# Performance work log

Hardware: AMD Instinct MI355X
Metric: run time of the kernel (lower is better)

Reference implementation:

```python
import jax, jax.numpy as jnp
import numpy as np

EMBED_DIM = 1024
NUM_HEADS = 16
HEAD_DIM = EMBED_DIM // NUM_HEADS
FF_DIM = 4 * EMBED_DIM
LN_EPS = 1e-5


def _layernorm(x, g, b):
    mu = jnp.mean(x, axis=-1, keepdims=True)
    var = jnp.var(x, axis=-1, keepdims=True)
    return (x - mu) * jax.lax.rsqrt(var + LN_EPS) * g + b


def setup_inputs() -> dict:
    key = jax.random.key(0)
    ks = jax.random.split(key, 8)
    B, T, C = 2, 2048, EMBED_DIM
    s_c = 1.0 / np.sqrt(C)
    s_f = 1.0 / np.sqrt(FF_DIM)
    return {
        "x": jax.random.normal(ks[0], (B, T, C), jnp.float32),
        "ln1_g": jnp.ones((C,), jnp.float32),
        "ln1_b": jnp.zeros((C,), jnp.float32),
        "qkv_w": jax.random.uniform(ks[1], (C, 3 * C), jnp.float32, -s_c, s_c),
        "qkv_b": jnp.zeros((3 * C,), jnp.float32),
        "out_w": jax.random.uniform(ks[2], (C, C), jnp.float32, -s_c, s_c),
        "out_b": jnp.zeros((C,), jnp.float32),
        "ln2_g": jnp.ones((C,), jnp.float32),
        "ln2_b": jnp.zeros((C,), jnp.float32),
        "ff1_w": jax.random.uniform(ks[3], (C, FF_DIM), jnp.float32, -s_c, s_c),
        "ff1_b": jnp.zeros((FF_DIM,), jnp.float32),
        "ff2_w": jax.random.uniform(ks[4], (FF_DIM, C), jnp.float32, -s_f, s_f),
        "ff2_b": jnp.zeros((C,), jnp.float32),
    }


def reference(x, ln1_g, ln1_b, qkv_w, qkv_b, out_w, out_b,
              ln2_g, ln2_b, ff1_w, ff1_b, ff2_w, ff2_b):
    B, T, C = x.shape
    H, D = NUM_HEADS, HEAD_DIM

    # --- pre-LN causal self-attention ---
    h = _layernorm(x, ln1_g, ln1_b)
    qkv = h @ qkv_w + qkv_b                      # [B,T,3C]
    q, k, v = jnp.split(qkv, 3, axis=-1)
    q = q.reshape(B, T, H, D)
    k = k.reshape(B, T, H, D)
    v = v.reshape(B, T, H, D)
    scores = jnp.einsum('bqhd,bkhd->bhqk', q, k) / np.sqrt(D)  # [B,H,T,T]
    causal = jnp.tril(jnp.ones((T, T), bool))
    scores = jnp.where(causal, scores, -jnp.inf)
    attn = jax.nn.softmax(scores, axis=-1)
    o = jnp.einsum('bhqk,bkhd->bqhd', attn, v).reshape(B, T, C)
    x = x + o @ out_w + out_b

    # --- GELU MLP ---
    h2 = _layernorm(x, ln2_g, ln2_b)
    ff = jax.nn.gelu(h2 @ ff1_w + ff1_b, approximate=False) @ ff2_w + ff2_b
    return x + ff
```

## Files before the change

### kernel.cpp

```cpp
#include <hip/hip_runtime.h>
#include <hip/hip_bf16.h>
#include <math.h>

#define B_ 2
#define T_ 2048
#define C_ 1024
#define H_ 16
#define D_ 64
#define F_ 4096
#define BT_ (B_*T_)

typedef __attribute__((ext_vector_type(8))) short bf16x8;
typedef __attribute__((ext_vector_type(4))) float f32x4;

__device__ __forceinline__ float bfraw2f(unsigned int u){
    union { unsigned int i; float f; } c; c.i = u << 16; return c.f;
}
__device__ __forceinline__ short f2bfraw(float f){
    union { float f; unsigned int i; } c; c.f = f;
    unsigned int u = c.i;
    u += 0x7fffu + ((u >> 16) & 1u);
    return (short)(u >> 16);
}
__device__ __forceinline__ void gl2lds16(const void* g, void* l) {
    __builtin_amdgcn_global_load_lds(
        (const __attribute__((address_space(1))) unsigned int*)g,
        (__attribute__((address_space(3))) unsigned int*)l,
        16, 0, 0);
}

__global__ __launch_bounds__(256) void wconv_t(const float* __restrict__ W,
                                               short* __restrict__ Wt,
                                               int K, int N)
{
    __shared__ short tile[64][65];
    int k0 = blockIdx.y * 64, n0 = blockIdx.x * 64;
    int t = threadIdx.x;
#pragma unroll
    for (int i = 0; i < 4; i++) {
        int idx = t + i * 256;
        int r = idx >> 4, c4 = (idx & 15) * 4;
        float4 u = *(const float4*)(W + (size_t)(k0 + r) * N + n0 + c4);
        tile[c4 + 0][r] = f2bfraw(u.x);
        tile[c4 + 1][r] = f2bfraw(u.y);
        tile[c4 + 2][r] = f2bfraw(u.z);
        tile[c4 + 3][r] = f2bfraw(u.w);
    }
    __syncthreads();
#pragma unroll
    for (int i = 0; i < 2; i++) {
        int idx = t + i * 256;
        int r = idx >> 3, c8 = (idx & 7) * 8;
        short v[8];
#pragma unroll
        for (int u8 = 0; u8 < 8; u8++) v[u8] = tile[r][c8 + u8];
        *(uint4*)(Wt + (size_t)(n0 + r) * K + k0 + c8) = *(const uint4*)v;
    }
}

__global__ __launch_bounds__(256) void v_transpose(const __hip_bfloat16* __restrict__ qkv,
                                                   short* __restrict__ vt)
{
    __shared__ short tile[64][65];
    int kb = blockIdx.x * 64;
    int h = blockIdx.y, b = blockIdx.z;
    const short* src = (const short*)qkv + (size_t)b * T_ * 3 * C_ + 2 * C_ + h * D_;
    int t = threadIdx.x;
#pragma unroll
    for (int i = 0; i < 2; i++) {
        int idx = t + i * 256;
        int r = idx >> 3, c8 = (idx & 7) * 8;
        bf16x8 v = *(const bf16x8*)(src + (size_t)(kb + r) * 3 * C_ + c8);
#pragma unroll
        for (int u = 0; u < 8; u++) tile[c8 + u][r] = v[u];
    }
    __syncthreads();
    short* dst = vt + (size_t)(b * H_ + h) * D_ * T_ + kb;
#pragma unroll
    for (int i = 0; i < 2; i++) {
        int idx = t + i * 256;
        int r = idx >> 3, c8 = (idx & 7) * 8;
        short v[8];
#pragma unroll
        for (int u = 0; u < 8; u++) v[u] = tile[r][c8 + u];
        *(uint4*)(dst + (size_t)r * T_ + c8) = *(const uint4*)v;
    }
}

__global__ __launch_bounds__(256) void ln_fused(const float* __restrict__ x, int ldx,
                                                const float* __restrict__ g,
                                                const float* __restrict__ b,
                                                __hip_bfloat16* out, int ldo)
{
    __shared__ float sm1[4], sm2[4];
    __shared__ float smu, srs;
    int row = blockIdx.x, t = threadIdx.x;
    const float* xr = x + (size_t)row * ldx;
    float v[4]; float s = 0.f, ss = 0.f;
#pragma unroll
    for (int i = 0; i < 4; i++) {
        float f = xr[t + i * 256];
        v[i] = f; s += f; ss += f * f;
    }
#pragma unroll
    for (int off = 32; off >= 1; off >>= 1) {
        s  += __shfl_xor(s,  off);
        ss += __shfl_xor(ss, off);
    }
    int wave = t >> 6, lane = t & 63;
    if (!lane) { sm1[wave] = s; sm2[wave] = ss; }
    __syncthreads();
    if (t == 0) {
        s  = sm1[0] + sm1[1] + sm1[2] + sm1[3];
        ss = sm2[0] + sm2[1] + sm2[2] + sm2[3];
        float mu  = s * (1.f / C_);
        float var = ss * (1.f / C_) - mu * mu;
        if (var < 0.f) var = 0.f;
        smu = mu; srs = rsqrtf(var + 1e-5f);
    }
    __syncthreads();
    float mu = smu, rs = srs;
#pragma unroll
    for (int i = 0; i < 4; i++) {
        int c = t + i * 256;
        out[(size_t)row * ldo + c] = __float2bfloat16((v[i] - mu) * rs * g[c] + b[c]);
    }
}

template<int ACT>
__global__ __launch_bounds__(256) void gemm128(
    const __hip_bfloat16* A, int lda,
    const short* Wt, int ldw, int noff, int koff,
    const float* __restrict__ bias, int boff,
    void* out, int ldo,
    int K)
{
    __shared__ __align__(16) short As[2][128 * 32];
    __shared__ __align__(16) short Bs[2][128 * 32];
    int tid = threadIdx.x;
    int w = tid >> 6, lane = tid & 63;
    int quad = lane >> 4, l16 = lane & 15;
    int wm = w >> 1, wn = w & 1;
    int m0 = blockIdx.y * 128, n0 = blockIdx.x * 128;
    int lr = lane >> 2, lk = (lane & 3) * 8;

    const __hip_bfloat16* Ag = A + (size_t)(m0 + w * 32 + lr) * lda + lk;
    const short*          Bg = Wt + (size_t)(noff + n0 + w * 32 + lr) * ldw + koff + lk;

    f32x4 acc[4][4];
#pragma unroll
    for (int i = 0; i < 4; i++)
#pragma unroll
        for (int j = 0; j < 4; j++) acc[i][j] = (f32x4){0.f, 0.f, 0.f, 0.f};

    gl2lds16(Ag,            &As[0][(w * 32) * 32]);
    gl2lds16(Ag + 16 * lda, &As[0][(w * 32 + 16) * 32]);
    gl2lds16(Bg,            &Bs[0][(w * 32) * 32]);
    gl2lds16(Bg + 16 * ldw, &Bs[0][(w * 32 + 16) * 32]);
    __syncthreads();

    int cur = 0;
    for (int k0 = 0; k0 < K; k0 += 32) {
        if (k0 + 32 < K) {
            int kn = k0 + 32, nb = cur ^ 1;
            gl2lds16(Ag + kn,            &As[nb][(w * 32) * 32]);
            gl2lds16(Ag + 16 * lda + kn, &As[nb][(w * 32 + 16) * 32]);
            gl2lds16(Bg + kn,            &Bs[nb][(w * 32) * 32]);
            gl2lds16(Bg + 16 * ldw + kn, &Bs[nb][(w * 32 + 16) * 32]);
        }
        bf16x8 af[4], bfr[4];
#pragma unroll
        for (int mt = 0; mt < 4; mt++)
            af[mt] = *(const bf16x8*)&As[cur][(wm * 64 + mt * 16 + l16) * 32 + quad * 8];
#pragma unroll
        for (int nt = 0; nt < 4; nt++)
            bfr[nt] = *(const bf16x8*)&Bs[cur][(wn * 64 + nt * 16 + l16) * 32 + quad * 8];
#pragma unroll
        for (int mt = 0; mt < 4; mt++)
#pragma unroll
            for (int nt = 0; nt < 4; nt++)
                acc[mt][nt] = __builtin_amdgcn_mfma_f32_16x16x32_bf16(af[mt], bfr[nt], acc[mt][nt], 0, 0, 0);
        __syncthreads();
        cur ^= 1;
    }

#pragma unroll
    for (int nt = 0; nt < 4; nt++) {
        int c = n0 + wn * 64 + nt * 16 + l16;
        float bv = bias ? bias[boff + c] : 0.f;
#pragma unroll
        for (int mt = 0; mt < 4; mt++) {
#pragma unroll
            for (int reg = 0; reg < 4; reg++) {
                int r = m0 + wm * 64 + mt * 16 + quad * 4 + reg;
                float v = acc[mt][nt][reg] + bv;
                if (ACT == 1) v = 0.5f * v * (1.f + erff(v * 0.70710678118654752f));
                ((__hip_bfloat16*)out)[(size_t)r * ldo + c] = __float2bfloat16(v);
            }
        }
    }
}

__global__ __launch_bounds__(256) void gemm64n(
    const __hip_bfloat16* A, int lda,
    const short* Wt, int ldw, int koff,
    const float* __restrict__ bias,
    const float* res, int ldres,
    float* out, int ldo,
    int K)
{
    __shared__ __align__(16) short As[2][128 * 32];
    __shared__ __align__(16) short Bs[2][64 * 32];
    int tid = threadIdx.x;
    int w = tid >> 6, lane = tid & 63;
    int quad = lane >> 4, l16 = lane & 15;
    int wm = w >> 1, wn = w & 1;
    int m0 = blockIdx.y * 128, n0 = blockIdx.x * 64;
    int lr = lane >> 2, lk = (lane & 3) * 8;

    const __hip_bfloat16* Ag = A + (size_t)(m0 + w * 32 + lr) * lda + lk;
    const short*          Bg = Wt + (size_t)(n0 + w * 16 + lr) * ldw + koff + lk;

    f32x4 acc[4][2];
#pragma unroll
    for (int i = 0; i < 4; i++)
#pragma unroll
        for (int j = 0; j < 2; j++) acc[i][j] = (f32x4){0.f, 0.f, 0.f, 0.f};

    gl2lds16(Ag,            &As[0][(w * 32) * 32]);
    gl2lds16(Ag + 16 * lda, &As[0][(w * 32 + 16) * 32]);
    gl2lds16(Bg,            &Bs[0][(w * 16) * 32]);
    __syncthreads();

    int cur = 0;
    for (int k0 = 0; k0 < K; k0 += 32) {
        if (k0 + 32 < K) {
            int kn = k0 + 32, nb = cur ^ 1;
            gl2lds16(Ag + kn,            &As[nb][(w * 32) * 32]);
            gl2lds16(Ag + 16 * lda + kn, &As[nb][(w * 32 + 16) * 32]);
            gl2lds16(Bg + kn,            &Bs[nb][(w * 16) * 32]);
        }
        bf16x8 af[4], bfr[2];
#pragma unroll
        for (int mt = 0; mt < 4; mt++)
            af[mt] = *(const bf16x8*)&As[cur][(wm * 64 + mt * 16 + l16) * 32 + quad * 8];
#pragma unroll
        for (int nt = 0; nt < 2; nt++)
            bfr[nt] = *(const bf16x8*)&Bs[cur][(wn * 32 + nt * 16 + l16) * 32 + quad * 8];
#pragma unroll
        for (int mt = 0; mt < 4; mt++)
#pragma unroll
            for (int nt = 0; nt < 2; nt++)
                acc[mt][nt] = __builtin_amdgcn_mfma_f32_16x16x32_bf16(af[mt], bfr[nt], acc[mt][nt], 0, 0, 0);
        __syncthreads();
        cur ^= 1;
    }

#pragma unroll
    for (int nt = 0; nt < 2; nt++) {
        int c = n0 + wn * 32 + nt * 16 + l16;
        float bv = bias ? bias[c] : 0.f;
#pragma unroll
        for (int mt = 0; mt < 4; mt++) {
#pragma unroll
            for (int reg = 0; reg < 4; reg++) {
                int r = m0 + wm * 64 + mt * 16 + quad * 4 + reg;
                float v = acc[mt][nt][reg] + bv + res[(size_t)r * ldres + c];
                out[(size_t)r * ldo + c] = v;
            }
        }
    }
}

__global__ __launch_bounds__(256, 2) void attn_flash(__hip_bfloat16* qkv,
                                                     const short* __restrict__ vt)
{
    __shared__ __align__(16) short Ks[2][64 * 64];
    __shared__ __align__(16) short Vs[2][64 * 64];
    __shared__ __align__(16) short Pl[4][16 * 72];
    int tid = threadIdx.x;
    int wave = tid >> 6, lane = tid & 63;
    int quad = lane >> 4, l16 = lane & 15;
    int fid = blockIdx.x + 16 * blockIdx.y;
    int h = (fid & 7) * 2 + ((fid >> 3) >> 4);
    int i = (fid >> 3) & 15;
    int b = blockIdx.z;
    int qbs[2]; qbs[0] = i; qbs[1] = 31 - i;
    const size_t rs = 3 * C_;
    __hip_bfloat16* base = qkv + (size_t)b * T_ * rs;
    const __hip_bfloat16* Qb = base + h * D_;
    const __hip_bfloat16* Kb = base + C_ + h * D_;
    const short* Vt = vt + (size_t)(b * H_ + h) * D_ * T_;

    bf16x8 qf[2][2];
#pragma unroll
    for (int tq = 0; tq < 2; tq++) {
        const __hip_bfloat16* qr = Qb + (size_t)(qbs[tq] * 64 + wave * 16 + l16) * rs + quad * 8;
        qf[tq][0] = *(const bf16x8*)qr;
        qf[tq][1] = *(const bf16x8*)(qr + 32);
    }

    f32x4 o[2][4];
    float m[2][4], l[2][4];
#pragma unroll
    for (int tq = 0; tq < 2; tq++)
#pragma unroll
        for (int t = 0; t < 4; t++) {
            o[tq][t] = (f32x4){0.f, 0.f, 0.f, 0.f};
            m[tq][t] = -INFINITY;
            l[tq][t] = 0.f;
        }
    short* Pw = &Pl[wave][0];

    int srow = wave * 16 + (lane >> 3);
    int scg  = ((lane & 7) ^ (lane >> 3)) * 8;
    const __hip_bfloat16* Kg = Kb + (size_t)srow * rs + scg;
    const short*          Vg = Vt + (size_t)srow * T_ + scg;

    int cur = 0;
#pragma unroll
    for (int j = 0; j < 2; j++) {
        gl2lds16(Kg + (size_t)(j * 8) * rs, &Ks[0][(wave * 2 + j) * 512]);
        gl2lds16(Vg + (size_t)(j * 8) * T_, &Vs[0][(wave * 2 + j) * 512]);
    }
    __syncthreads();

    int qhi = qbs[1];
    int swz = (l16 & 7);
    for (int kt = 0; kt <= qhi; kt++) {
        if (kt < qhi) {
            int kb = (kt + 1) * 64;
#pragma unroll
            for (int j = 0; j < 2; j++) {
                gl2lds16(Kg + (size_t)(kb + j * 8) * rs, &Ks[cur ^ 1][(wave * 2 + j) * 512]);
                gl2lds16(Vg + (size_t)(j * 8) * T_ + kb, &Vs[cur ^ 1][(wave * 2 + j) * 512]);
            }
        }
        const short* Kc = Ks[cur];
        const short* Vc = Vs[cur];
#pragma unroll
        for (int tq = 0; tq < 2; tq++) {
            if (tq == 0 && kt > qbs[0]) continue;
            f32x4 sa[4];
            __builtin_amdgcn_s_setprio(1);
#pragma unroll
            for (int t16 = 0; t16 < 4; t16++) {
                int row = t16 * 16 + l16;
                bf16x8 kf0 = *(const bf16x8*)&Kc[row * 64 + ((quad     ^ swz)) * 8];
                bf16x8 kf1 = *(const bf16x8*)&Kc[row * 64 + (((quad + 4) ^ swz)) * 8];
                f32x4 s = (f32x4){0.f, 0.f, 0.f, 0.f};
                s = __builtin_amdgcn_mfma_f32_16x16x32_bf16(qf[tq][0], kf0, s, 0, 0, 0);
                s = __builtin_amdgcn_mfma_f32_16x16x32_bf16(qf[tq][1], kf1, s, 0, 0, 0);
                sa[t16] = s;
            }
            __builtin_amdgcn_s_setprio(0);
            bool maskit = (kt == qbs[tq]);
#pragma unroll
            for (int t16 = 0; t16 < 4; t16++) {
#pragma unroll
                for (int reg = 0; reg < 4; reg++) {
                    float v = sa[t16][reg] * 0.125f;
                    if (maskit) {
                        int keyl = t16 * 16 + l16;
                        int ql = wave * 16 + quad * 4 + reg;
                        if (keyl > ql) v = -3.0e38f;
                    }
                    sa[t16][reg] = v;
                }
            }
            float mx[4];
#pragma unroll
            for (int reg = 0; reg < 4; reg++)
                mx[reg] = fmaxf(fmaxf(sa[0][reg], sa[1][reg]), fmaxf(sa[2][reg], sa[3][reg]));
#pragma unroll
            for (int off = 8; off >= 1; off >>= 1)
#pragma unroll
                for (int reg = 0; reg < 4; reg++)
                    mx[reg] = fmaxf(mx[reg], __shfl_xor(mx[reg], off));
            float alpha[4];
#pragma unroll
            for (int reg = 0; reg < 4; reg++) {
                float mn = fmaxf(m[tq][reg], mx[reg]);
                alpha[reg] = __expf(m[tq][reg] - mn);
                m[tq][reg] = mn;
            }
            float rsum[4] = {0.f, 0.f, 0.f, 0.f};
#pragma unroll
            for (int t16 = 0; t16 < 4; t16++) {
#pragma unroll
                for (int reg = 0; reg < 4; reg++) {
                    float p = __expf(sa[t16][reg] - m[tq][reg]);
                    rsum[reg] += p;
                    Pw[(quad * 4 + reg) * 72 + t16 * 16 + l16] = f2bfraw(p);
                }
            }
#pragma unroll
            for (int off = 8; off >= 1; off >>= 1)
#pragma unroll
                for (int reg = 0; reg < 4; reg++)
                    rsum[reg] += __shfl_xor(rsum[reg], off);
#pragma unroll
            for (int reg = 0; reg < 4; reg++)
                l[tq][reg] = l[tq][reg] * alpha[reg] + rsum[reg];
#pragma unroll
            for (int t = 0; t < 4; t++)
#pragma unroll
                for (int reg = 0; reg < 4; reg++)
                    o[tq][t][reg] *= alpha[reg];
            __builtin_amdgcn_s_setprio(1);
#pragma unroll
            for (int chunk = 0; chunk < 2; chunk++) {
                bf16x8 pf = *(const bf16x8*)&Pw[l16 * 72 + chunk * 32 + quad * 8];
#pragma unroll
                for (int dt = 0; dt < 4; dt++) {
                    int row = dt * 16 + l16;
                    bf16x8 vf = *(const bf16x8*)&Vc[row * 64 + (((chunk * 4 + quad) ^ swz)) * 8];
                    o[tq][dt] = __builtin_amdgcn_mfma_f32_16x16x32_bf16(pf, vf, o[tq][dt], 0, 0, 0);
                }
            }
            __builtin_amdgcn_s_setprio(0);
        }
        __syncthreads();
        cur ^= 1;
    }

#pragma unroll
    for (int tq = 0; tq < 2; tq++) {
#pragma unroll
        for (int dt = 0; dt < 4; dt++) {
#pragma unroll
            for (int reg = 0; reg < 4; reg++) {
                int r = qbs[tq] * 64 + wave * 16 + quad * 4 + reg;
                float v = o[tq][dt][reg] / l[tq][reg];
                base[(size_t)r * rs + h * D_ + dt * 16 + l16] = __float2bfloat16(v);
            }
        }
    }
}

extern "C" void kernel_launch(void* const* d_in, const int* in_sizes, int n_in,
                              void* d_out, int out_size, void* d_ws, size_t ws_size,
                              hipStream_t stream)
{
    const float* x     = (const float*)d_in[0];
    const float* ln1_g = (const float*)d_in[1];
    const float* ln1_b = (const float*)d_in[2];
    const float* qkv_w = (const float*)d_in[3];
    const float* qkv_b = (const float*)d_in[4];
    const float* out_w = (const float*)d_in[5];
    const float* out_b = (const float*)d_in[6];
    const float* ln2_g = (const float*)d_in[7];
    const float* ln2_b = (const float*)d_in[8];
    const float* ff1_w = (const float*)d_in[9];
    const float* ff1_b = (const float*)d_in[10];
    const float* ff2_w = (const float*)d_in[11];
    const float* ff2_b = (const float*)d_in[12];

    char* ws = (char*)d_ws;
    __hip_bfloat16* qkv = (__hip_bfloat16*)ws;
    short* qkvwT = (short*)(ws + 25165824);
    short* outwT = (short*)(ws + 31457280);
    short* ff1wT = (short*)(ws + 33554432);
    short* ff2wT = (short*)(ws + 41943040);
    __hip_bfloat16* hbuf2 = qkv;
    __hip_bfloat16* act   = qkv + 1024;
    __hip_bfloat16* hbuf1 = (__hip_bfloat16*)d_out;
    float* x1 = (float*)d_out;
    short* vtbuf = (short*)d_out;

    wconv_t<<<dim3(3 * C_ / 64, C_ / 64), 256, 0, stream>>>(qkv_w, qkvwT, C_, 3 * C_);
    wconv_t<<<dim3(C_ / 64, C_ / 64),     256, 0, stream>>>(out_w, outwT, C_, C_);
    wconv_t<<<dim3(F_ / 64, C_ / 64),     256, 0, stream>>>(ff1_w, ff1wT, C_, F_);
    wconv_t<<<dim3(C_ / 64, F_ / 64),     256, 0, stream>>>(ff2_w, ff2wT, F_, C_);

    ln_fused<<<BT_, 256, 0, stream>>>(x, C_, ln1_g, ln1_b, hbuf1, C_);
    gemm128<0><<<dim3(3 * C_ / 128, BT_ / 128), 256, 0, stream>>>(
        hbuf1, C_, qkvwT, C_, 0, 0, qkv_b, 0, qkv, 3 * C_, C_);
    v_transpose<<<dim3(T_ / 64, H_, B_), 256, 0, stream>>>(qkv, vtbuf);
    attn_flash<<<dim3(16, H_, B_), 256, 0, stream>>>(qkv, vtbuf);
    gemm64n<<<dim3(C_ / 64, BT_ / 128), 256, 0, stream>>>(
        qkv, 3 * C_, outwT, C_, 0, out_b, x, C_, x1, C_, C_);
    ln_fused<<<BT_, 256, 0, stream>>>(x1, C_, ln2_g, ln2_b, hbuf2, 3 * C_);
    for (int f = 0; f < 2; f++) {
        gemm128<1><<<dim3(2048 / 128, BT_ / 128), 256, 0, stream>>>(
            hbuf2, 3 * C_, ff1wT, C_, f * 2048, 0, ff1_b, f * 2048,
            act, 3 * C_, C_);
        gemm64n<<<dim3(C_ / 64, BT_ / 128), 256, 0, stream>>>(
            act, 3 * C_, ff2wT, F_, f * 2048, (f == 0 ? ff2_b : nullptr),
            x1, C_, x1, C_, 2048);
    }
}
```

Baseline: 431.3 us.

## Triple-buffer GEMM LDS tiles with explicit vmcnt waits instead of syncthreads

Both GEMM kernels move from double to triple LDS buffering, prefetching two K-tiles ahead. Fine-grained s_waitcnt vmcnt counts plus raw s_barrier replace __syncthreads, so loads for later tiles stay in flight while the current tile is consumed. This is meant to hide global-to-LDS latency better. In exchange it raises LDS use per block, which may lower occupancy, and it depends on the vmcnt counts exactly matching the number of outstanding loads issued by gl2lds16.

```diff
diff --git a/kernel.cpp b/kernel.cpp
--- a/kernel.cpp
+++ b/kernel.cpp
@@ -135,8 +135,8 @@
     void* out, int ldo,
     int K)
 {
-    __shared__ __align__(16) short As[2][128 * 32];
-    __shared__ __align__(16) short Bs[2][128 * 32];
+    __shared__ __align__(16) short As[3][128 * 32];
+    __shared__ __align__(16) short Bs[3][128 * 32];
     int tid = threadIdx.x;
     int w = tid >> 6, lane = tid & 63;
     int quad = lane >> 4, l16 = lane & 15;
@@ -153,21 +153,37 @@
 #pragma unroll
         for (int j = 0; j < 4; j++) acc[i][j] = (f32x4){0.f, 0.f, 0.f, 0.f};
 
-    gl2lds16(Ag,            &As[0][(w * 32) * 32]);
-    gl2lds16(Ag + 16 * lda, &As[0][(w * 32 + 16) * 32]);
-    gl2lds16(Bg,            &Bs[0][(w * 32) * 32]);
-    gl2lds16(Bg + 16 * ldw, &Bs[0][(w * 32 + 16) * 32]);
-    __syncthreads();
+    const int NT = K >> 5;
+    {
+        gl2lds16(Ag,            &As[0][(w * 32) * 32]);
+        gl2lds16(Ag + 16 * lda, &As[0][(w * 32 + 16) * 32]);
+        gl2lds16(Bg,            &Bs[0][(w * 32) * 32]);
+        gl2lds16(Bg + 16 * ldw, &Bs[0][(w * 32 + 16) * 32]);
+        if (NT > 1) {
+            gl2lds16(Ag + 32,            &As[1][(w * 32) * 32]);
+            gl2lds16(Ag + 16 * lda + 32, &As[1][(w * 32 + 16) * 32]);
+            gl2lds16(Bg + 32,            &Bs[1][(w * 32) * 32]);
+            gl2lds16(Bg + 16 * ldw + 32, &Bs[1][(w * 32 + 16) * 32]);
+        }
+    }
 
     int cur = 0;
-    for (int k0 = 0; k0 < K; k0 += 32) {
-        if (k0 + 32 < K) {
-            int kn = k0 + 32, nb = cur ^ 1;
-            gl2lds16(Ag + kn,            &As[nb][(w * 32) * 32]);
-            gl2lds16(Ag + 16 * lda + kn, &As[nb][(w * 32 + 16) * 32]);
-            gl2lds16(Bg + kn,            &Bs[nb][(w * 32) * 32]);
-            gl2lds16(Bg + 16 * ldw + kn, &Bs[nb][(w * 32 + 16) * 32]);
-        }
+    for (int t = 0; t < NT; t++) {
+        if (t + 2 < NT) {
+            int sb = cur + 2; if (sb >= 3) sb -= 3;
+            int ko = (t + 2) << 5;
+            gl2lds16(Ag + ko,            &As[sb][(w * 32) * 32]);
+            gl2lds16(Ag + 16 * lda + ko, &As[sb][(w * 32 + 16) * 32]);
+            gl2lds16(Bg + ko,            &Bs[sb][(w * 32) * 32]);
+            gl2lds16(Bg + 16 * ldw + ko, &Bs[sb][(w * 32 + 16) * 32]);
+        }
+        int ahead = NT - 1 - t;
+        if (ahead >= 2)      asm volatile("s_waitcnt vmcnt(8)" ::: "memory");
+        else if (ahead == 1) asm volatile("s_waitcnt vmcnt(4)" ::: "memory");
+        else                 asm volatile("s_waitcnt vmcnt(0)" ::: "memory");
+        __builtin_amdgcn_s_barrier();
+        __builtin_amdgcn_sched_barrier(0);
+
         bf16x8 af[4], bfr[4];
 #pragma unroll
         for (int mt = 0; mt < 4; mt++)
@@ -180,8 +196,10 @@
 #pragma unroll
             for (int nt = 0; nt < 4; nt++)
                 acc[mt][nt] = __builtin_amdgcn_mfma_f32_16x16x32_bf16(af[mt], bfr[nt], acc[mt][nt], 0, 0, 0);
-        __syncthreads();
-        cur ^= 1;
+
+        __builtin_amdgcn_sched_barrier(0);
+        __builtin_amdgcn_s_barrier();
+        cur = (cur == 2) ? 0 : cur + 1;
     }
 
 #pragma unroll
@@ -209,8 +227,8 @@
     float* out, int ldo,
     int K)
 {
-    __shared__ __align__(16) short As[2][128 * 32];
-    __shared__ __align__(16) short Bs[2][64 * 32];
+    __shared__ __align__(16) short As[3][128 * 32];
+    __shared__ __align__(16) short Bs[3][64 * 32];
     int tid = threadIdx.x;
     int w = tid >> 6, lane = tid & 63;
     int quad = lane >> 4, l16 = lane & 15;
@@ -227,19 +245,34 @@
 #pragma unroll
         for (int j = 0; j < 2; j++) acc[i][j] = (f32x4){0.f, 0.f, 0.f, 0.f};
 
-    gl2lds16(Ag,            &As[0][(w * 32) * 32]);
-    gl2lds16(Ag + 16 * lda, &As[0][(w * 32 + 16) * 32]);
-    gl2lds16(Bg,            &Bs[0][(w * 16) * 32]);
-    __syncthreads();
+    const int NT = K >> 5;
+    {
+        gl2lds16(Ag,            &As[0][(w * 32) * 32]);
+        gl2lds16(Ag + 16 * lda, &As[0][(w * 32 + 16) * 32]);
+        gl2lds16(Bg,            &Bs[0][(w * 16) * 32]);
+        if (NT > 1) {
+            gl2lds16(Ag + 32,            &As[1][(w * 32) * 32]);
+            gl2lds16(Ag + 16 * lda + 32, &As[1][(w * 32 + 16) * 32]);
+            gl2lds16(Bg + 32,            &Bs[1][(w * 16) * 32]);
+        }
+    }
 
     int cur = 0;
-    for (int k0 = 0; k0 < K; k0 += 32) {
-        if (k0 + 32 < K) {
-            int kn = k0 + 32, nb = cur ^ 1;
-            gl2lds16(Ag + kn,            &As[nb][(w * 32) * 32]);
-            gl2lds16(Ag + 16 * lda + kn, &As[nb][(w * 32 + 16) * 32]);
-            gl2lds16(Bg + kn,            &Bs[nb][(w * 16) * 32]);
-        }
+    for (int t = 0; t < NT; t++) {
+        if (t + 2 < NT) {
+            int sb = cur + 2; if (sb >= 3) sb -= 3;
+            int ko = (t + 2) << 5;
+            gl2lds16(Ag + ko,            &As[sb][(w * 32) * 32]);
+            gl2lds16(Ag + 16 * lda + ko, &As[sb][(w * 32 + 16) * 32]);
+            gl2lds16(Bg + ko,            &Bs[sb][(w * 16) * 32]);
+        }
+        int ahead = NT - 1 - t;
+        if (ahead >= 2)      asm volatile("s_waitcnt vmcnt(6)" ::: "memory");
+        else if (ahead == 1) asm volatile("s_waitcnt vmcnt(3)" ::: "memory");
+        else                 asm volatile("s_waitcnt vmcnt(0)" ::: "memory");
+        __builtin_amdgcn_s_barrier();
+        __builtin_amdgcn_sched_barrier(0);
+
         bf16x8 af[4], bfr[2];
 #pragma unroll
         for (int mt = 0; mt < 4; mt++)
@@ -252,8 +285,10 @@
 #pragma unroll
             for (int nt = 0; nt < 2; nt++)
                 acc[mt][nt] = __builtin_amdgcn_mfma_f32_16x16x32_bf16(af[mt], bfr[nt], acc[mt][nt], 0, 0, 0);
-        __syncthreads();
-        cur ^= 1;
+
+        __builtin_amdgcn_sched_barrier(0);
+        __builtin_amdgcn_s_barrier();
+        cur = (cur == 2) ? 0 : cur + 1;
     }
 
 #pragma unroll
```

Measured after the change: 431.5 us. About the same (+0.0%).
